# Performance work log

Hardware: AMD Instinct MI355X
Metric: run time of the kernel (lower is better)

## Reference

```python
import jax, jax.numpy as jnp
import numpy as np

N = 131072      # H*W*batch = 128*128*8 features
D = 256         # feature_dim
P = 64          # proj_dim
E = 260096      # (2*H*W - H - W)*batch edges of the grid graph
G = 8192        # number of groups
SIM_THRESHOLD = 0.5


def setup_inputs() -> dict:
    key = jax.random.key(0)
    k0, k1, k2, k3 = jax.random.split(key, 4)
    features = jax.random.normal(k0, (N, D), dtype=jnp.float32)
    proj_W = jax.random.normal(k1, (D, P), dtype=jnp.float32) / np.sqrt(D)
    edge_index = jax.random.randint(k2, (2, E), 0, N, dtype=jnp.int64)
    group_ids = jax.random.randint(k3, (N,), 0, G, dtype=jnp.int64)
    return {
        "features": features,
        "proj_W": proj_W,
        "edge_index": edge_index,
        "group_ids": group_ids,
        "num_groups": G,
    }


def reference(features, proj_W, edge_index, group_ids, num_groups):
    # Projection: [N, D] @ [D, P] -> [N, P]
    proj = features @ proj_W
    # Pair comparison: gather both endpoints per edge, dot product per edge
    src, dst = edge_index[0], edge_index[1]
    sims = jnp.sum(proj[src] * proj[dst], axis=-1)            # [E]
    edge_logits = jax.nn.sigmoid(sims - SIM_THRESHOLD)        # [E]
    # Group mean pooling: scatter-add features per group, divide by size
    ones = jnp.ones((features.shape[0],), dtype=features.dtype)
    group_sums = jax.ops.segment_sum(features, group_ids, num_segments=num_groups)  # [G, D]
    group_sizes = jax.ops.segment_sum(ones, group_ids, num_segments=num_groups)     # [G]
    group_sizes = jnp.maximum(group_sizes, 1.0)
    group_means = group_sums / group_sizes[:, None]           # [G, D]
    return group_means, edge_logits
```

## Files before the change

kernel.cpp:

```cpp
#include <hip/hip_runtime.h>
#include <math.h>

constexpr int Nn = 131072;
constexpr int Dd = 256;
constexpr int Pp = 64;
constexpr int Gg = 8192;
constexpr int Ee = 260096;
constexpr int CAP = 64;
constexpr float SIM_TH = 0.5f;

typedef _Float16 half8 __attribute__((ext_vector_type(8)));
typedef _Float16 half4 __attribute__((ext_vector_type(4)));
typedef float floatx4 __attribute__((ext_vector_type(4)));


__global__ __launch_bounds__(256) void k_AB(
    const float* __restrict__ A,
    const float* __restrict__ W,
    _Float16* __restrict__ proj,
    const int* __restrict__ gid,
    int* __restrict__ cursor,
    int* __restrict__ bucket)
{
    if (blockIdx.x < 512) {
        const int i = blockIdx.x * 256 + threadIdx.x;
        const int g = gid[i];
        const int p = atomicAdd(&cursor[g], 1);
        if (p < CAP) bucket[g * CAP + p] = i;
        return;
    }

    __shared__ _Float16 WfL[16384];
    {
        const int t0 = threadIdx.x;
#pragma unroll
        for (int u = 0; u < 64; ++u) {
            const int i = t0 + 256 * u;
            const int j = i & 7;
            const int l = (i >> 3) & 63;
            const int t = (i >> 9) & 3;
            const int c = i >> 11;
            const int k = c * 32 + (l >> 4) * 8 + j;
            const int n = t * 16 + (l & 15);
            WfL[i] = (_Float16)W[k * Pp + n];
        }
    }
    __syncthreads();

    const int blk = blockIdx.x - 512;
    const int l = threadIdx.x & 63;
    const int w = threadIdx.x >> 6;
    const int rowbase = blk * 64 + w * 16;
    const int am = l & 15;
    const int q  = l >> 4;

    const float* __restrict__ arow = A + (size_t)(rowbase + am) * Dd + q * 8;
    const half8* __restrict__ bfrag = reinterpret_cast<const half8*>(WfL) + l;

    floatx4 acc[4];
#pragma unroll
    for (int t = 0; t < 4; ++t) acc[t] = (floatx4){0.f, 0.f, 0.f, 0.f};

#pragma unroll
    for (int c = 0; c < 8; ++c) {
        const float4 fa = *reinterpret_cast<const float4*>(arow + c * 32);
        const float4 fb = *reinterpret_cast<const float4*>(arow + c * 32 + 4);
        half8 a;
        a[0] = (_Float16)fa.x; a[1] = (_Float16)fa.y;
        a[2] = (_Float16)fa.z; a[3] = (_Float16)fa.w;
        a[4] = (_Float16)fb.x; a[5] = (_Float16)fb.y;
        a[6] = (_Float16)fb.z; a[7] = (_Float16)fb.w;
        const half8 b0 = bfrag[(c * 4 + 0) * 64];
        const half8 b1 = bfrag[(c * 4 + 1) * 64];
        const half8 b2 = bfrag[(c * 4 + 2) * 64];
        const half8 b3 = bfrag[(c * 4 + 3) * 64];
        acc[0] = __builtin_amdgcn_mfma_f32_16x16x32_f16(a, b0, acc[0], 0, 0, 0);
        acc[1] = __builtin_amdgcn_mfma_f32_16x16x32_f16(a, b1, acc[1], 0, 0, 0);
        acc[2] = __builtin_amdgcn_mfma_f32_16x16x32_f16(a, b2, acc[2], 0, 0, 0);
        acc[3] = __builtin_amdgcn_mfma_f32_16x16x32_f16(a, b3, acc[3], 0, 0, 0);
    }

#pragma unroll
    for (int r = 0; r < 4; ++r) {
        half4 h;
        h[0] = (_Float16)acc[0][r];
        h[1] = (_Float16)acc[1][r];
        h[2] = (_Float16)acc[2][r];
        h[3] = (_Float16)acc[3][r];
        *reinterpret_cast<half4*>(
            proj + (size_t)(rowbase + q * 4 + r) * Pp + am * 4) = h;
    }
}

__global__ __launch_bounds__(256) void k_CD(
    const float* __restrict__ features,
    const int* __restrict__ bucket,
    const int* __restrict__ cnt,
    float* __restrict__ out_means,
    const _Float16* __restrict__ proj,
    const int* __restrict__ ei,
    float* __restrict__ out_logits)
{
    if (blockIdx.x < 4096) {
        __shared__ float4 part[2][2][64];

        const int lane = threadIdx.x & 63;
        const int w    = threadIdx.x >> 6;
        const int gs   = w >> 1;
        const int half = w & 1;
        const int g = blockIdx.x * 2 + gs;
        const int n = min(cnt[g], CAP);
        const int col = lane * 4;
        const int* __restrict__ bk = bucket + g * CAP;

        float4 s = make_float4(0.f, 0.f, 0.f, 0.f);
        int k = half;
        for (; k + 14 < n; k += 16) {
            int r[8];
#pragma unroll
            for (int u = 0; u < 8; ++u) r[u] = bk[k + 2 * u];
            float4 f[8];
#pragma unroll
            for (int u = 0; u < 8; ++u)
                f[u] = *reinterpret_cast<const float4*>(features + (size_t)r[u] * Dd + col);
#pragma unroll
            for (int u = 0; u < 8; ++u) {
                s.x += f[u].x; s.y += f[u].y; s.z += f[u].z; s.w += f[u].w;
            }
        }
        for (; k < n; k += 2) {
            const float4 f = *reinterpret_cast<const float4*>(features + (size_t)bk[k] * Dd + col);
            s.x += f.x; s.y += f.y; s.z += f.z; s.w += f.w;
        }
        part[gs][half][lane] = s;
        __syncthreads();

        if (half == 0) {
            const float4 o = part[gs][1][lane];
            s.x += o.x; s.y += o.y; s.z += o.z; s.w += o.w;
            const float inv = 1.0f / (float)max(n, 1);
            s.x *= inv; s.y *= inv; s.z *= inv; s.w *= inv;
            *reinterpret_cast<float4*>(out_means + (size_t)g * Dd + col) = s;
        }
        return;
    }

    const int bid = blockIdx.x - 4096;
    const int sub = threadIdx.x & 7;
    const int sg  = bid * 32 + (threadIdx.x >> 3);
    const int e0  = sg * 4;

    int s[4], t[4];
#pragma unroll
    for (int u = 0; u < 4; ++u) { s[u] = ei[e0 + u]; t[u] = ei[Ee + e0 + u]; }

    half8 a[4], b[4];
#pragma unroll
    for (int u = 0; u < 4; ++u) {
        a[u] = *reinterpret_cast<const half8*>(proj + (size_t)s[u] * Pp + sub * 8);
        b[u] = *reinterpret_cast<const half8*>(proj + (size_t)t[u] * Pp + sub * 8);
    }

    float v[4];
#pragma unroll
    for (int u = 0; u < 4; ++u) {
        float acc = 0.f;
#pragma unroll
        for (int j = 0; j < 8; ++j)
            acc = fmaf((float)a[u][j], (float)b[u][j], acc);
        v[u] = acc;
    }

#pragma unroll
    for (int off = 4; off >= 1; off >>= 1) {
#pragma unroll
        for (int u = 0; u < 4; ++u) v[u] += __shfl_xor(v[u], off, 64);
    }

    if (sub < 4) {
        const float x = v[sub];
        out_logits[e0 + sub] = 1.0f / (1.0f + __expf(-(x - SIM_TH)));
    }
}

extern "C" void kernel_launch(void* const* d_in, const int* in_sizes, int n_in,
                              void* d_out, int out_size, void* d_ws, size_t ws_size,
                              hipStream_t stream)
{
    const float* features = (const float*)d_in[0];
    const float* W        = (const float*)d_in[1];
    const int*   ei       = (const int*)d_in[2];
    const int*   gid      = (const int*)d_in[3];

    float* out_means  = (float*)d_out;
    float* out_logits = out_means + (size_t)Gg * Dd;

    _Float16*  proj    = (_Float16*)d_ws;
    int*       bucket  = (int*)(proj + (size_t)Nn * Pp);
    int*       cursor  = bucket + Gg * CAP;

    hipMemsetAsync(cursor, 0, (size_t)Gg * sizeof(int), stream);

    hipLaunchKernelGGL(k_AB, dim3(512 + Nn / 64), dim3(256), 0, stream,
                       features, W, proj, gid, cursor, bucket);
    hipLaunchKernelGGL(k_CD, dim3(4096 + Ee / 128), dim3(256), 0, stream,
                       features, bucket, cursor, out_means,
                       proj, ei, out_logits);
}
```

Baseline: 246.3 us.

## Pre-convert W once, replace memset, double rows per GEMM block

```diff
diff --git a/kernel.cpp b/kernel.cpp
--- a/kernel.cpp
+++ b/kernel.cpp
@@ -14,9 +14,25 @@
 typedef float floatx4 __attribute__((ext_vector_type(4)));
 
 
+__global__ __launch_bounds__(256) void k_prep(
+    const float* __restrict__ W,
+    _Float16* __restrict__ Wf,
+    int* __restrict__ cursor)
+{
+    const int i = blockIdx.x * 256 + threadIdx.x;
+    const int j = i & 7;
+    const int l = (i >> 3) & 63;
+    const int t = (i >> 9) & 3;
+    const int c = i >> 11;
+    const int k = c * 32 + (l >> 4) * 8 + j;
+    const int n = t * 16 + (l & 15);
+    Wf[i] = (_Float16)W[k * Pp + n];
+    if (i < Gg) cursor[i] = 0;
+}
+
 __global__ __launch_bounds__(256) void k_AB(
     const float* __restrict__ A,
-    const float* __restrict__ W,
+    const _Float16* __restrict__ Wf,
     _Float16* __restrict__ proj,
     const int* __restrict__ gid,
     int* __restrict__ cursor,
@@ -32,17 +48,12 @@
 
     __shared__ _Float16 WfL[16384];
     {
-        const int t0 = threadIdx.x;
-#pragma unroll
-        for (int u = 0; u < 64; ++u) {
-            const int i = t0 + 256 * u;
-            const int j = i & 7;
-            const int l = (i >> 3) & 63;
-            const int t = (i >> 9) & 3;
-            const int c = i >> 11;
-            const int k = c * 32 + (l >> 4) * 8 + j;
-            const int n = t * 16 + (l & 15);
-            WfL[i] = (_Float16)W[k * Pp + n];
+        const float4* __restrict__ src = reinterpret_cast<const float4*>(Wf);
+        float4* dst = reinterpret_cast<float4*>(WfL);
+#pragma unroll
+        for (int u = 0; u < 8; ++u) {
+            const int idx = threadIdx.x + 256 * u;
+            dst[idx] = src[idx];
         }
     }
     __syncthreads();
@@ -50,45 +61,65 @@
     const int blk = blockIdx.x - 512;
     const int l = threadIdx.x & 63;
     const int w = threadIdx.x >> 6;
-    const int rowbase = blk * 64 + w * 16;
+    const int rowbase = blk * 128 + w * 32;
     const int am = l & 15;
     const int q  = l >> 4;
 
-    const float* __restrict__ arow = A + (size_t)(rowbase + am) * Dd + q * 8;
+    const float* __restrict__ a0p = A + (size_t)(rowbase + am) * Dd + q * 8;
+    const float* __restrict__ a1p = a0p + 16 * Dd;
     const half8* __restrict__ bfrag = reinterpret_cast<const half8*>(WfL) + l;
 
-    floatx4 acc[4];
-#pragma unroll
-    for (int t = 0; t < 4; ++t) acc[t] = (floatx4){0.f, 0.f, 0.f, 0.f};
+    floatx4 acc0[4], acc1[4];
+#pragma unroll
+    for (int t = 0; t < 4; ++t) {
+        acc0[t] = (floatx4){0.f, 0.f, 0.f, 0.f};
+        acc1[t] = (floatx4){0.f, 0.f, 0.f, 0.f};
+    }
 
 #pragma unroll
     for (int c = 0; c < 8; ++c) {
-        const float4 fa = *reinterpret_cast<const float4*>(arow + c * 32);
-        const float4 fb = *reinterpret_cast<const float4*>(arow + c * 32 + 4);
-        half8 a;
-        a[0] = (_Float16)fa.x; a[1] = (_Float16)fa.y;
-        a[2] = (_Float16)fa.z; a[3] = (_Float16)fa.w;
-        a[4] = (_Float16)fb.x; a[5] = (_Float16)fb.y;
-        a[6] = (_Float16)fb.z; a[7] = (_Float16)fb.w;
+        const float4 fa0 = *reinterpret_cast<const float4*>(a0p + c * 32);
+        const float4 fb0 = *reinterpret_cast<const float4*>(a0p + c * 32 + 4);
+        const float4 fa1 = *reinterpret_cast<const float4*>(a1p + c * 32);
+        const float4 fb1 = *reinterpret_cast<const float4*>(a1p + c * 32 + 4);
         const half8 b0 = bfrag[(c * 4 + 0) * 64];
         const half8 b1 = bfrag[(c * 4 + 1) * 64];
         const half8 b2 = bfrag[(c * 4 + 2) * 64];
         const half8 b3 = bfrag[(c * 4 + 3) * 64];
-        acc[0] = __builtin_amdgcn_mfma_f32_16x16x32_f16(a, b0, acc[0], 0, 0, 0);
-        acc[1] = __builtin_amdgcn_mfma_f32_16x16x32_f16(a, b1, acc[1], 0, 0, 0);
-        acc[2] = __builtin_amdgcn_mfma_f32_16x16x32_f16(a, b2, acc[2], 0, 0, 0);
-        acc[3] = __builtin_amdgcn_mfma_f32_16x16x32_f16(a, b3, acc[3], 0, 0, 0);
+        half8 a0, a1;
+        a0[0] = (_Float16)fa0.x; a0[1] = (_Float16)fa0.y;
+        a0[2] = (_Float16)fa0.z; a0[3] = (_Float16)fa0.w;
+        a0[4] = (_Float16)fb0.x; a0[5] = (_Float16)fb0.y;
+        a0[6] = (_Float16)fb0.z; a0[7] = (_Float16)fb0.w;
+        a1[0] = (_Float16)fa1.x; a1[1] = (_Float16)fa1.y;
+        a1[2] = (_Float16)fa1.z; a1[3] = (_Float16)fa1.w;
+        a1[4] = (_Float16)fb1.x; a1[5] = (_Float16)fb1.y;
+        a1[6] = (_Float16)fb1.z; a1[7] = (_Float16)fb1.w;
+        acc0[0] = __builtin_amdgcn_mfma_f32_16x16x32_f16(a0, b0, acc0[0], 0, 0, 0);
+        acc0[1] = __builtin_amdgcn_mfma_f32_16x16x32_f16(a0, b1, acc0[1], 0, 0, 0);
+        acc0[2] = __builtin_amdgcn_mfma_f32_16x16x32_f16(a0, b2, acc0[2], 0, 0, 0);
+        acc0[3] = __builtin_amdgcn_mfma_f32_16x16x32_f16(a0, b3, acc0[3], 0, 0, 0);
+        acc1[0] = __builtin_amdgcn_mfma_f32_16x16x32_f16(a1, b0, acc1[0], 0, 0, 0);
+        acc1[1] = __builtin_amdgcn_mfma_f32_16x16x32_f16(a1, b1, acc1[1], 0, 0, 0);
+        acc1[2] = __builtin_amdgcn_mfma_f32_16x16x32_f16(a1, b2, acc1[2], 0, 0, 0);
+        acc1[3] = __builtin_amdgcn_mfma_f32_16x16x32_f16(a1, b3, acc1[3], 0, 0, 0);
     }
 
 #pragma unroll
     for (int r = 0; r < 4; ++r) {
-        half4 h;
-        h[0] = (_Float16)acc[0][r];
-        h[1] = (_Float16)acc[1][r];
-        h[2] = (_Float16)acc[2][r];
-        h[3] = (_Float16)acc[3][r];
+        half4 h0, h1;
+        h0[0] = (_Float16)acc0[0][r];
+        h0[1] = (_Float16)acc0[1][r];
+        h0[2] = (_Float16)acc0[2][r];
+        h0[3] = (_Float16)acc0[3][r];
+        h1[0] = (_Float16)acc1[0][r];
+        h1[1] = (_Float16)acc1[1][r];
+        h1[2] = (_Float16)acc1[2][r];
+        h1[3] = (_Float16)acc1[3][r];
         *reinterpret_cast<half4*>(
-            proj + (size_t)(rowbase + q * 4 + r) * Pp + am * 4) = h;
+            proj + (size_t)(rowbase + q * 4 + r) * Pp + am * 4) = h0;
+        *reinterpret_cast<half4*>(
+            proj + (size_t)(rowbase + 16 + q * 4 + r) * Pp + am * 4) = h1;
     }
 }
 
@@ -198,11 +229,11 @@
     _Float16*  proj    = (_Float16*)d_ws;
     int*       bucket  = (int*)(proj + (size_t)Nn * Pp);
     int*       cursor  = bucket + Gg * CAP;
-
-    hipMemsetAsync(cursor, 0, (size_t)Gg * sizeof(int), stream);
-
-    hipLaunchKernelGGL(k_AB, dim3(512 + Nn / 64), dim3(256), 0, stream,
-                       features, W, proj, gid, cursor, bucket);
+    _Float16*  Wf      = (_Float16*)(cursor + Gg);
+
+    hipLaunchKernelGGL(k_prep, dim3(64), dim3(256), 0, stream, W, Wf, cursor);
+    hipLaunchKernelGGL(k_AB, dim3(512 + Nn / 128), dim3(256), 0, stream,
+                       features, Wf, proj, gid, cursor, bucket);
     hipLaunchKernelGGL(k_CD, dim3(4096 + Ee / 128), dim3(256), 0, stream,
                        features, bucket, cursor, out_means,
                        proj, ei, out_logits);
```

After: 239.4 us, median of 2. 1.03x faster.
